# Kernel tuning notes

Measured on AMD Instinct MI355X. Metric: run time of the kernel, lower is better.

The kernel has to match this reference:

```python
import jax, jax.numpy as jnp
import numpy as np

N_NODES = 100000
N_EDGES = 1600000
N_GRAPHS = 512
IN_DIM = 128
HID = 128


def setup_inputs() -> dict:
    key = jax.random.key(0)
    ks = jax.random.split(key, 8)
    x = jax.random.normal(ks[0], (N_NODES, IN_DIM), dtype=jnp.float32)
    edge_index = jax.random.randint(ks[1], (2, N_EDGES), 0, N_NODES, dtype=jnp.int64)
    batch = jnp.sort(jax.random.randint(ks[2], (N_NODES,), 0, N_GRAPHS, dtype=jnp.int64))
    s1 = 1.0 / np.sqrt(IN_DIM)
    s2 = 1.0 / np.sqrt(HID)
    W1 = jax.random.normal(ks[3], (IN_DIM, HID), dtype=jnp.float32) * s1
    b1 = jnp.zeros((HID,), dtype=jnp.float32)
    W2 = jax.random.normal(ks[4], (HID, HID), dtype=jnp.float32) * s2
    b2 = jnp.zeros((HID,), dtype=jnp.float32)
    Wp = jax.random.normal(ks[5], (HID, 1), dtype=jnp.float32) * s2
    bp = jnp.zeros((1,), dtype=jnp.float32)
    return {"x": x, "edge_index": edge_index, "batch": batch,
            "W1": W1, "b1": b1, "W2": W2, "b2": b2, "Wp": Wp, "bp": bp}


def _gcn_conv(x, W, b, src, dst, deg_inv_sqrt):
    # PyG GCNConv: linear transform, then normalized scatter-add (self-loops
    # already appended to src/dst), then bias.
    h = x @ W                                   # [N, H]
    norm = deg_inv_sqrt[src] * deg_inv_sqrt[dst]  # [E+N]
    msg = h[src] * norm[:, None]                # gather + scale
    out = jax.ops.segment_sum(msg, dst, num_segments=N_NODES)
    return out + b


def reference(x, edge_index, batch, W1, b1, W2, b2, Wp, bp):
    # Add self-loops once; degree (with self-loops) over target nodes.
    si = jnp.arange(N_NODES, dtype=edge_index.dtype)
    src = jnp.concatenate([edge_index[0], si])
    dst = jnp.concatenate([edge_index[1], si])
    ones = jnp.ones(src.shape[0], dtype=x.dtype)
    deg = jax.ops.segment_sum(ones, dst, num_segments=N_NODES)
    deg_inv_sqrt = jnp.where(deg > 0, jax.lax.rsqrt(jnp.maximum(deg, 1.0)), 0.0)

    h = jax.nn.relu(_gcn_conv(x, W1, b1, src, dst, deg_inv_sqrt))  # dropout = identity (eval)
    h = jax.nn.relu(_gcn_conv(h, W2, b2, src, dst, deg_inv_sqrt))

    # global_mean_pool over graph ids
    sums = jax.ops.segment_sum(h, batch, num_segments=N_GRAPHS)
    cnts = jax.ops.segment_sum(jnp.ones(N_NODES, dtype=h.dtype), batch, num_segments=N_GRAPHS)
    pooled = sums / jnp.maximum(cnts, 1.0)[:, None]               # [G, H]

    return (pooled @ Wp + bp).squeeze(-1)                          # [G]
```

## Files before the change

kernel.cpp:

```cpp
#include <hip/hip_runtime.h>
#include <hip/hip_bf16.h>

#define NN 100000
#define NG 512
#define H  128

typedef _Float16 half8 __attribute__((ext_vector_type(8)));
typedef float f32x4 __attribute__((ext_vector_type(4)));

__global__ __launch_bounds__(256) void k_wprep_hist(const float* __restrict__ W1,
                                                    const float* __restrict__ W2,
                                                    _Float16* __restrict__ Wt1,
                                                    _Float16* __restrict__ Wt2,
                                                    const int* __restrict__ dst,
                                                    int* __restrict__ deg, int E) {
    int bb = blockIdx.x;
    if (bb < 128) {
        const float* W = (bb < 64) ? W1 : W2;
        _Float16* Wt = (bb < 64) ? Wt1 : Wt2;
        int i = (bb & 63) * 256 + threadIdx.x;
        int k = i >> 7, n = i & 127;
        Wt[n * 128 + k] = (_Float16)W[i];
        return;
    }
    int e = (bb - 128) * 256 + threadIdx.x;
    if (e < E) atomicAdd(&deg[dst[e]], 1);
}

__global__ __launch_bounds__(256) void k_scan_block(const int* __restrict__ deg,
                                                    int* __restrict__ rowptr,
                                                    int* __restrict__ bsum, int n) {
    __shared__ int s[256];
    int tid = threadIdx.x;
    int i = blockIdx.x * 256 + tid;
    int v = (i < n) ? deg[i] : 0;
    s[tid] = v;
    __syncthreads();
    #pragma unroll
    for (int off = 1; off < 256; off <<= 1) {
        int t = (tid >= off) ? s[tid - off] : 0;
        __syncthreads();
        s[tid] += t;
        __syncthreads();
    }
    if (i < n) rowptr[i] = s[tid] - v;
    if (tid == 255) bsum[blockIdx.x] = s[255];
}

__global__ __launch_bounds__(512) void k_scan_top(int* __restrict__ bsum, int nb) {
    __shared__ int s[512];
    int tid = threadIdx.x;
    int v = (tid < nb) ? bsum[tid] : 0;
    s[tid] = v;
    __syncthreads();
    #pragma unroll
    for (int off = 1; off < 512; off <<= 1) {
        int t = (tid >= off) ? s[tid - off] : 0;
        __syncthreads();
        s[tid] += t;
        __syncthreads();
    }
    if (tid < nb) bsum[tid] = s[tid] - v;
}

__global__ __launch_bounds__(256) void k_scan_fin(int* __restrict__ rowptr,
                                                  const int* __restrict__ bsum,
                                                  const int* __restrict__ deg,
                                                  int* __restrict__ cursor,
                                                  float* __restrict__ dinv,
                                                  int n, int E) {
    int i = blockIdx.x * 256 + threadIdx.x;
    if (i >= n) return;
    int r = rowptr[i] + bsum[i >> 8];
    rowptr[i] = r;
    cursor[i] = r;
    dinv[i] = rsqrtf((float)deg[i] + 1.0f);
    if (i == 0) rowptr[n] = E;
}

__global__ __launch_bounds__(256) void k_fill_gemm1(
        const int* __restrict__ src, const int* __restrict__ dst,
        int* __restrict__ cursor, int* __restrict__ col, int E, int nfb,
        const float* __restrict__ x, const _Float16* __restrict__ Wt1,
        const float* __restrict__ dinv, _Float16* __restrict__ tS, int n) {
    if ((int)blockIdx.x < nfb) {
        int e = blockIdx.x * 256 + threadIdx.x;
        if (e >= E) return;
        int d = dst[e];
        int pos = atomicAdd(&cursor[d], 1);
        col[pos] = src[e];
        return;
    }
    const int row0 = ((int)blockIdx.x - nfb) * 64;
    const int tid = threadIdx.x;
    const int w = tid >> 6, lane = tid & 63;
    const int l16 = lane & 15, quad = lane >> 4;
    const int Arow = row0 + w * 16 + l16;
    f32x4 acc[8] = {};
    #pragma unroll
    for (int kk = 0; kk < 4; ++kk) {
        half8 af;
        if (Arow < n) {
            const float* ap = x + (size_t)Arow * H + kk * 32 + quad * 8;
            float4 a0 = ((const float4*)ap)[0];
            float4 a1 = ((const float4*)ap)[1];
            af[0] = (_Float16)a0.x; af[1] = (_Float16)a0.y;
            af[2] = (_Float16)a0.z; af[3] = (_Float16)a0.w;
            af[4] = (_Float16)a1.x; af[5] = (_Float16)a1.y;
            af[6] = (_Float16)a1.z; af[7] = (_Float16)a1.w;
        } else {
            #pragma unroll
            for (int j = 0; j < 8; ++j) af[j] = (_Float16)0.0f;
        }
        #pragma unroll
        for (int nt = 0; nt < 8; ++nt) {
            half8 bf = *((const half8*)(Wt1 + (nt * 16 + l16) * H + kk * 32 + quad * 8));
            acc[nt] = __builtin_amdgcn_mfma_f32_16x16x32_f16(af, bf, acc[nt], 0, 0, 0);
        }
    }
    #pragma unroll
    for (int r = 0; r < 4; ++r) {
        int R = row0 + w * 16 + quad * 4 + r;
        if (R < n) {
            float sc = dinv[R];
            _Float16* crow = tS + (size_t)R * H + l16;
            #pragma unroll
            for (int nt = 0; nt < 8; ++nt)
                crow[nt * 16] = (_Float16)(acc[nt][r] * sc);
        }
    }
}

__global__ __launch_bounds__(256) void k_gemm2(const _Float16* __restrict__ h1,
                                               const _Float16* __restrict__ Wt2,
                                               const float* __restrict__ dinv,
                                               _Float16* __restrict__ tS2, int n) {
    const int row0 = blockIdx.x * 64;
    const int tid = threadIdx.x;
    const int w = tid >> 6, lane = tid & 63;
    const int l16 = lane & 15, quad = lane >> 4;
    const int Arow = row0 + w * 16 + l16;
    f32x4 acc[8] = {};
    #pragma unroll
    for (int kk = 0; kk < 4; ++kk) {
        half8 af;
        if (Arow < n) {
            af = ((const half8*)(h1 + (size_t)Arow * H))[kk * 4 + quad];
        } else {
            #pragma unroll
            for (int j = 0; j < 8; ++j) af[j] = (_Float16)0.0f;
        }
        #pragma unroll
        for (int nt = 0; nt < 8; ++nt) {
            half8 bf = *((const half8*)(Wt2 + (nt * 16 + l16) * H + kk * 32 + quad * 8));
            acc[nt] = __builtin_amdgcn_mfma_f32_16x16x32_f16(af, bf, acc[nt], 0, 0, 0);
        }
    }
    #pragma unroll
    for (int r = 0; r < 4; ++r) {
        int R = row0 + w * 16 + quad * 4 + r;
        if (R < n) {
            float sc = dinv[R];
            _Float16* crow = tS2 + (size_t)R * H + l16;
            #pragma unroll
            for (int nt = 0; nt < 8; ++nt)
                crow[nt * 16] = (_Float16)(acc[nt][r] * sc);
        }
    }
}

__device__ __forceinline__ half8 ld_row16_nol1(const _Float16* p) {
    union { unsigned long long u[2]; half8 h; } t;
    const unsigned long long* q = (const unsigned long long*)p;
    t.u[0] = __hip_atomic_load(q,     __ATOMIC_RELAXED, __HIP_MEMORY_SCOPE_AGENT);
    t.u[1] = __hip_atomic_load(q + 1, __ATOMIC_RELAXED, __HIP_MEMORY_SCOPE_AGENT);
    return t.h;
}

template <bool NOL1>
__device__ __forceinline__ void gather_rows_h(const _Float16* __restrict__ tS,
                                              const int* __restrict__ col,
                                              int node, int e0, int end,
                                              float acc[8]) {
    const int lane = threadIdx.x & 63;
    const int q = lane >> 4;
    const int l16 = lane & 15;
    float a0[8] = {}, a1[8] = {};
    if (q == 0) {
        half8 v = ((const half8*)tS)[(size_t)node * 16 + l16];
        #pragma unroll
        for (int i = 0; i < 8; ++i) a0[i] = (float)v[i];
    }
    for (int base = e0; base < end; base += 64) {
        int ce = base + lane;
        int cidx = (ce < end) ? col[ce] : 0;
        int m = min(64, end - base);
        int nf = m >> 2;
        int g = 0;
        for (; g + 2 <= nf; g += 2) {
            int s0 = __shfl(cidx, 4 * g + q);
            int s1 = __shfl(cidx, 4 * g + 4 + q);
            half8 v0, v1;
            if (NOL1) {
                v0 = ld_row16_nol1(tS + (size_t)s0 * H + l16 * 8);
                v1 = ld_row16_nol1(tS + (size_t)s1 * H + l16 * 8);
            } else {
                v0 = ((const half8*)tS)[(size_t)s0 * 16 + l16];
                v1 = ((const half8*)tS)[(size_t)s1 * 16 + l16];
            }
            #pragma unroll
            for (int i = 0; i < 8; ++i) {
                a0[i] += (float)v0[i];
                a1[i] += (float)v1[i];
            }
        }
        if (g < nf) {
            int s0 = __shfl(cidx, 4 * g + q);
            half8 v0 = NOL1 ? ld_row16_nol1(tS + (size_t)s0 * H + l16 * 8)
                            : ((const half8*)tS)[(size_t)s0 * 16 + l16];
            #pragma unroll
            for (int i = 0; i < 8; ++i) a0[i] += (float)v0[i];
        }
        int tail = m & 3;
        if (tail) {
            int s = __shfl(cidx, 4 * nf + q);
            if (q < tail) {
                half8 v = NOL1 ? ld_row16_nol1(tS + (size_t)s * H + l16 * 8)
                               : ((const half8*)tS)[(size_t)s * 16 + l16];
                #pragma unroll
                for (int i = 0; i < 8; ++i) a0[i] += (float)v[i];
            }
        }
    }
    #pragma unroll
    for (int i = 0; i < 8; ++i) {
        float t = a0[i] + a1[i];
        t += __shfl_xor(t, 16);
        t += __shfl_xor(t, 32);
        acc[i] = t;
    }
}

__global__ __launch_bounds__(256) void k_gather1(const _Float16* __restrict__ tS,
                                                 const int* __restrict__ rowptr,
                                                 const int* __restrict__ col,
                                                 const float* __restrict__ dinv,
                                                 const float* __restrict__ b,
                                                 _Float16* __restrict__ out, int n) {
    int node = blockIdx.x * 4 + (threadIdx.x >> 6);
    int lane = threadIdx.x & 63;
    int q = lane >> 4, l16 = lane & 15;
    if (node >= n) return;
    int e0 = rowptr[node], end = rowptr[node + 1];
    float acc[8];
    gather_rows_h<false>(tS, col, node, e0, end, acc);
    if (q == 0) {
        float dn = dinv[node];
        const float4* b4 = (const float4*)b;
        float4 bb0 = b4[2 * l16], bb1 = b4[2 * l16 + 1];
        half8 hv;
        hv[0] = (_Float16)fmaxf(dn * acc[0] + bb0.x, 0.0f);
        hv[1] = (_Float16)fmaxf(dn * acc[1] + bb0.y, 0.0f);
        hv[2] = (_Float16)fmaxf(dn * acc[2] + bb0.z, 0.0f);
        hv[3] = (_Float16)fmaxf(dn * acc[3] + bb0.w, 0.0f);
        hv[4] = (_Float16)fmaxf(dn * acc[4] + bb1.x, 0.0f);
        hv[5] = (_Float16)fmaxf(dn * acc[5] + bb1.y, 0.0f);
        hv[6] = (_Float16)fmaxf(dn * acc[6] + bb1.z, 0.0f);
        hv[7] = (_Float16)fmaxf(dn * acc[7] + bb1.w, 0.0f);
        ((half8*)out)[(size_t)node * 16 + l16] = hv;
    }
}

__global__ __launch_bounds__(256) void k_gather2(const _Float16* __restrict__ tS,
                                                 const int* __restrict__ rowptr,
                                                 const int* __restrict__ col,
                                                 const float* __restrict__ dinv,
                                                 const float* __restrict__ b,
                                                 const float* __restrict__ Wp,
                                                 const int* __restrict__ batch,
                                                 float* __restrict__ pool,
                                                 float* __restrict__ cnt, int n) {
    int node = blockIdx.x * 4 + (threadIdx.x >> 6);
    int lane = threadIdx.x & 63;
    int l16 = lane & 15;
    if (node >= n) return;
    int e0 = rowptr[node], end = rowptr[node + 1];
    float acc[8];
    gather_rows_h<true>(tS, col, node, e0, end, acc);
    float dn = dinv[node];
    const float4* b4 = (const float4*)b;
    const float4* w4 = (const float4*)Wp;
    float4 bb0 = b4[2 * l16], bb1 = b4[2 * l16 + 1];
    float4 wp0 = w4[2 * l16], wp1 = w4[2 * l16 + 1];
    float s = fmaxf(dn * acc[0] + bb0.x, 0.0f) * wp0.x +
              fmaxf(dn * acc[1] + bb0.y, 0.0f) * wp0.y +
              fmaxf(dn * acc[2] + bb0.z, 0.0f) * wp0.z +
              fmaxf(dn * acc[3] + bb0.w, 0.0f) * wp0.w +
              fmaxf(dn * acc[4] + bb1.x, 0.0f) * wp1.x +
              fmaxf(dn * acc[5] + bb1.y, 0.0f) * wp1.y +
              fmaxf(dn * acc[6] + bb1.z, 0.0f) * wp1.z +
              fmaxf(dn * acc[7] + bb1.w, 0.0f) * wp1.w;
    s += __shfl_xor(s, 1);
    s += __shfl_xor(s, 2);
    s += __shfl_xor(s, 4);
    s += __shfl_xor(s, 8);
    if (lane == 0) {
        int g = batch[node];
        atomicAdd(&pool[g], s);
        atomicAdd(&cnt[g], 1.0f);
    }
}

__global__ __launch_bounds__(256) void final_out_kernel(const float* __restrict__ pool,
                                                        const float* __restrict__ cnt,
                                                        const float* __restrict__ bp,
                                                        float* __restrict__ out, int g) {
    int i = blockIdx.x * 256 + threadIdx.x;
    if (i < g) out[i] = pool[i] / fmaxf(cnt[i], 1.0f) + bp[0];
}

extern "C" void kernel_launch(void* const* d_in, const int* in_sizes, int n_in,
                              void* d_out, int out_size, void* d_ws, size_t ws_size,
                              hipStream_t stream) {
    const float* x     = (const float*)d_in[0];
    const int*   ei    = (const int*)d_in[1];
    const int*   batch = (const int*)d_in[2];
    const float* W1    = (const float*)d_in[3];
    const float* b1    = (const float*)d_in[4];
    const float* W2    = (const float*)d_in[5];
    const float* b2    = (const float*)d_in[6];
    const float* Wp    = (const float*)d_in[7];
    const float* bp    = (const float*)d_in[8];
    float* out = (float*)d_out;

    const int E = in_sizes[1] / 2;
    const int* src = ei;
    const int* dst = ei + E;

    const size_t BUFH = (size_t)NN * H * sizeof(_Float16);
    const size_t NI   = 401408;
    char* ws = (char*)d_ws;
    size_t off = 0;
    _Float16* tS   = (_Float16*)(ws + off); off += BUFH;
    _Float16* h1   = (_Float16*)(ws + off); off += BUFH;
    _Float16* tS2  = (_Float16*)(ws + off); off += BUFH;
    int*      deg  = (int*)     (ws + off); off += NI;
    int*   rowptr  = (int*)     (ws + off); off += NI;
    int*   cursor  = (int*)     (ws + off); off += NI;
    float*    dinv = (float*)   (ws + off); off += NI;
    int*      col  = (int*)     (ws + off); off += ((size_t)E * 4 + 4095) / 4096 * 4096;
    _Float16* Wt1  = (_Float16*)(ws + off); off += 32768;
    _Float16* Wt2  = (_Float16*)(ws + off); off += 32768;
    int*      bsum = (int*)     (ws + off); off += 4096;
    float*    pool = (float*)   (ws + off); off += 2048;
    float*    cnt  = (float*)   (ws + off); off += 2048;

    const int NB  = (NN + 255) / 256;
    const int NFB = (E + 255) / 256;
    const int NGB = (NN + 63) / 64;

    hipMemsetAsync(deg, 0, NN * sizeof(int), stream);
    hipMemsetAsync(pool, 0, 4096, stream);
    k_wprep_hist<<<128 + NFB, 256, 0, stream>>>(W1, W2, Wt1, Wt2, dst, deg, E);
    k_scan_block<<<NB, 256, 0, stream>>>(deg, rowptr, bsum, NN);
    k_scan_top<<<1, 512, 0, stream>>>(bsum, NB);
    k_scan_fin<<<NB, 256, 0, stream>>>(rowptr, bsum, deg, cursor, dinv, NN, E);

    k_fill_gemm1<<<NFB + NGB, 256, 0, stream>>>(src, dst, cursor, col, E, NFB,
                                                x, Wt1, dinv, tS, NN);

    k_gather1<<<(NN + 3) / 4, 256, 0, stream>>>(tS, rowptr, col, dinv, b1, h1, NN);
    k_gemm2<<<NGB, 256, 0, stream>>>(h1, Wt2, dinv, tS2, NN);

    k_gather2<<<(NN + 3) / 4, 256, 0, stream>>>(tS2, rowptr, col, dinv, b2, Wp,
                                                batch, pool, cnt, NN);

    final_out_kernel<<<(NG + 255) / 256, 256, 0, stream>>>(pool, cnt, bp, out, NG);
}
```

Measured before the change: 663.1 us.

## Unroll gather by four rows, use 32-bit offsets, compute graph counts by binary search

Measured after the change: 728.7 us. +9.9%, slower.

```diff
diff --git a/kernel.cpp b/kernel.cpp
--- a/kernel.cpp
+++ b/kernel.cpp
@@ -169,7 +169,7 @@
     }
 }
 
-__device__ __forceinline__ half8 ld_row16_nol1(const _Float16* p) {
+__device__ __forceinline__ half8 ld_row16_nol1(const void* p) {
     union { unsigned long long u[2]; half8 h; } t;
     const unsigned long long* q = (const unsigned long long*)p;
     t.u[0] = __hip_atomic_load(q,     __ATOMIC_RELAXED, __HIP_MEMORY_SCOPE_AGENT);
@@ -185,9 +185,11 @@
     const int lane = threadIdx.x & 63;
     const int q = lane >> 4;
     const int l16 = lane & 15;
+    const char* tSb = (const char*)tS;
+    const uint32_t fo = (uint32_t)(l16 << 4);
     float a0[8] = {}, a1[8] = {};
     if (q == 0) {
-        half8 v = ((const half8*)tS)[(size_t)node * 16 + l16];
+        half8 v = *(const half8*)(tSb + (((uint32_t)node << 8) + fo));
         #pragma unroll
         for (int i = 0; i < 8; ++i) a0[i] = (float)v[i];
     }
@@ -195,40 +197,29 @@
         int ce = base + lane;
         int cidx = (ce < end) ? col[ce] : 0;
         int m = min(64, end - base);
-        int nf = m >> 2;
-        int g = 0;
-        for (; g + 2 <= nf; g += 2) {
-            int s0 = __shfl(cidx, 4 * g + q);
-            int s1 = __shfl(cidx, 4 * g + 4 + q);
-            half8 v0, v1;
+        int ng = (m + 3) >> 2;
+        for (int g = 0; g < ng; g += 4) {
+            int p0 = 4 * g + q, p1 = p0 + 4, p2 = p0 + 8, p3 = p0 + 12;
+            int s0 = __shfl(cidx, p0), s1 = __shfl(cidx, p1);
+            int s2 = __shfl(cidx, p2), s3 = __shfl(cidx, p3);
+            half8 v0 = {}, v1 = {}, v2 = {}, v3 = {};
             if (NOL1) {
-                v0 = ld_row16_nol1(tS + (size_t)s0 * H + l16 * 8);
-                v1 = ld_row16_nol1(tS + (size_t)s1 * H + l16 * 8);
+                if (p0 < m) v0 = ld_row16_nol1(tSb + (((uint32_t)s0 << 8) + fo));
+                if (p1 < m) v1 = ld_row16_nol1(tSb + (((uint32_t)s1 << 8) + fo));
+                if (p2 < m) v2 = ld_row16_nol1(tSb + (((uint32_t)s2 << 8) + fo));
+                if (p3 < m) v3 = ld_row16_nol1(tSb + (((uint32_t)s3 << 8) + fo));
             } else {
-                v0 = ((const half8*)tS)[(size_t)s0 * 16 + l16];
-                v1 = ((const half8*)tS)[(size_t)s1 * 16 + l16];
+                if (p0 < m) v0 = *(const half8*)(tSb + (((uint32_t)s0 << 8) + fo));
+                if (p1 < m) v1 = *(const half8*)(tSb + (((uint32_t)s1 << 8) + fo));
+                if (p2 < m) v2 = *(const half8*)(tSb + (((uint32_t)s2 << 8) + fo));
+                if (p3 < m) v3 = *(const half8*)(tSb + (((uint32_t)s3 << 8) + fo));
             }
             #pragma unroll
             for (int i = 0; i < 8; ++i) {
                 a0[i] += (float)v0[i];
                 a1[i] += (float)v1[i];
-            }
-        }
-        if (g < nf) {
-            int s0 = __shfl(cidx, 4 * g + q);
-            half8 v0 = NOL1 ? ld_row16_nol1(tS + (size_t)s0 * H + l16 * 8)
-                            : ((const half8*)tS)[(size_t)s0 * 16 + l16];
-            #pragma unroll
-            for (int i = 0; i < 8; ++i) a0[i] += (float)v0[i];
-        }
-        int tail = m & 3;
-        if (tail) {
-            int s = __shfl(cidx, 4 * nf + q);
-            if (q < tail) {
-                half8 v = NOL1 ? ld_row16_nol1(tS + (size_t)s * H + l16 * 8)
-                               : ((const half8*)tS)[(size_t)s * 16 + l16];
-                #pragma unroll
-                for (int i = 0; i < 8; ++i) a0[i] += (float)v[i];
+                a0[i] += (float)v2[i];
+                a1[i] += (float)v3[i];
             }
         }
     }
@@ -278,8 +269,7 @@
                                                  const float* __restrict__ b,
                                                  const float* __restrict__ Wp,
                                                  const int* __restrict__ batch,
-                                                 float* __restrict__ pool,
-                                                 float* __restrict__ cnt, int n) {
+                                                 float* __restrict__ pool, int n) {
     int node = blockIdx.x * 4 + (threadIdx.x >> 6);
     int lane = threadIdx.x & 63;
     int l16 = lane & 15;
@@ -307,16 +297,22 @@
     if (lane == 0) {
         int g = batch[node];
         atomicAdd(&pool[g], s);
-        atomicAdd(&cnt[g], 1.0f);
     }
 }
 
 __global__ __launch_bounds__(256) void final_out_kernel(const float* __restrict__ pool,
-                                                        const float* __restrict__ cnt,
+                                                        const int* __restrict__ batch,
                                                         const float* __restrict__ bp,
                                                         float* __restrict__ out, int g) {
     int i = blockIdx.x * 256 + threadIdx.x;
-    if (i < g) out[i] = pool[i] / fmaxf(cnt[i], 1.0f) + bp[0];
+    if (i >= g) return;
+    int lo = 0, hi = NN;
+    while (lo < hi) { int mid = (lo + hi) >> 1; if (batch[mid] < i) lo = mid + 1; else hi = mid; }
+    int s0 = lo;
+    hi = NN;
+    while (lo < hi) { int mid = (lo + hi) >> 1; if (batch[mid] < i + 1) lo = mid + 1; else hi = mid; }
+    float c = (float)(lo - s0);
+    out[i] = pool[i] / fmaxf(c, 1.0f) + bp[0];
 }
 
 extern "C" void kernel_launch(void* const* d_in, const int* in_sizes, int n_in,
@@ -353,14 +349,13 @@
     _Float16* Wt2  = (_Float16*)(ws + off); off += 32768;
     int*      bsum = (int*)     (ws + off); off += 4096;
     float*    pool = (float*)   (ws + off); off += 2048;
-    float*    cnt  = (float*)   (ws + off); off += 2048;
 
     const int NB  = (NN + 255) / 256;
     const int NFB = (E + 255) / 256;
     const int NGB = (NN + 63) / 64;
 
     hipMemsetAsync(deg, 0, NN * sizeof(int), stream);
-    hipMemsetAsync(pool, 0, 4096, stream);
+    hipMemsetAsync(pool, 0, 2048, stream);
     k_wprep_hist<<<128 + NFB, 256, 0, stream>>>(W1, W2, Wt1, Wt2, dst, deg, E);
     k_scan_block<<<NB, 256, 0, stream>>>(deg, rowptr, bsum, NN);
     k_scan_top<<<1, 512, 0, stream>>>(bsum, NB);
@@ -373,7 +368,7 @@
     k_gemm2<<<NGB, 256, 0, stream>>>(h1, Wt2, dinv, tS2, NN);
 
     k_gather2<<<(NN + 3) / 4, 256, 0, stream>>>(tS2, rowptr, col, dinv, b2, Wp,
-                                                batch, pool, cnt, NN);
-
-    final_out_kernel<<<(NG + 255) / 256, 256, 0, stream>>>(pool, cnt, bp, out, NG);
-}
+                                                batch, pool, NN);
+
+    final_out_kernel<<<(NG + 255) / 256, 256, 0, stream>>>(pool, batch, bp, out, NG);
+}
```

## Split edge gathers into feature-column slices to shrink the random-access working set

Applied to the files above, without the earlier changes.

Result: slower. 1.530 ms (+130.7%).

```diff
diff --git a/kernel.cpp b/kernel.cpp
--- a/kernel.cpp
+++ b/kernel.cpp
@@ -5,7 +5,9 @@
 #define NG 512
 #define H  128
 
-typedef _Float16 half8 __attribute__((ext_vector_type(8)));
+typedef _Float16 half8  __attribute__((ext_vector_type(8)));
+typedef _Float16 half4v __attribute__((ext_vector_type(4)));
+typedef _Float16 half2v __attribute__((ext_vector_type(2)));
 typedef float f32x4 __attribute__((ext_vector_type(4)));
 
 __global__ __launch_bounds__(256) void k_wprep_hist(const float* __restrict__ W1,
@@ -169,27 +171,46 @@
     }
 }
 
-__device__ __forceinline__ half8 ld_row16_nol1(const _Float16* p) {
-    union { unsigned long long u[2]; half8 h; } t;
-    const unsigned long long* q = (const unsigned long long*)p;
-    t.u[0] = __hip_atomic_load(q,     __ATOMIC_RELAXED, __HIP_MEMORY_SCOPE_AGENT);
-    t.u[1] = __hip_atomic_load(q + 1, __ATOMIC_RELAXED, __HIP_MEMORY_SCOPE_AGENT);
-    return t.h;
-}
-
-template <bool NOL1>
-__device__ __forceinline__ void gather_rows_h(const _Float16* __restrict__ tS,
+template <int F, bool NOL1>
+__device__ __forceinline__ void frag_load(const char* p, float* t) {
+    if constexpr (F == 4) {
+        union { unsigned long long u; half4v h; } c;
+        if constexpr (NOL1) {
+            c.u = __hip_atomic_load((const unsigned long long*)p,
+                                    __ATOMIC_RELAXED, __HIP_MEMORY_SCOPE_AGENT);
+        } else {
+            c.h = *(const half4v*)p;
+        }
+        t[0] = (float)c.h[0]; t[1] = (float)c.h[1];
+        t[2] = (float)c.h[2]; t[3] = (float)c.h[3];
+    } else {
+        union { unsigned int u; half2v h; } c;
+        if constexpr (NOL1) {
+            c.u = __hip_atomic_load((const unsigned int*)p,
+                                    __ATOMIC_RELAXED, __HIP_MEMORY_SCOPE_AGENT);
+        } else {
+            c.h = *(const half2v*)p;
+        }
+        t[0] = (float)c.h[0]; t[1] = (float)c.h[1];
+    }
+}
+
+template <int F, bool NOL1>
+__device__ __forceinline__ void gather_rows_f(const _Float16* __restrict__ tS,
                                               const int* __restrict__ col,
-                                              int node, int e0, int end,
-                                              float acc[8]) {
+                                              int node, int e0, int end, int hoffB,
+                                              float acc[F]) {
     const int lane = threadIdx.x & 63;
     const int q = lane >> 4;
     const int l16 = lane & 15;
-    float a0[8] = {}, a1[8] = {};
+    const char* tSb = (const char*)tS;
+    const uint32_t fo = (uint32_t)(hoffB + l16 * (F * 2));
+    float a0[F] = {}, a1[F] = {};
     if (q == 0) {
-        half8 v = ((const half8*)tS)[(size_t)node * 16 + l16];
+        float t[F];
+        frag_load<F, false>(tSb + (((uint32_t)node << 8) + fo), t);
         #pragma unroll
-        for (int i = 0; i < 8; ++i) a0[i] = (float)v[i];
+        for (int i = 0; i < F; ++i) a0[i] = t[i];
     }
     for (int base = e0; base < end; base += 64) {
         int ce = base + lane;
@@ -200,40 +221,35 @@
         for (; g + 2 <= nf; g += 2) {
             int s0 = __shfl(cidx, 4 * g + q);
             int s1 = __shfl(cidx, 4 * g + 4 + q);
-            half8 v0, v1;
-            if (NOL1) {
-                v0 = ld_row16_nol1(tS + (size_t)s0 * H + l16 * 8);
-                v1 = ld_row16_nol1(tS + (size_t)s1 * H + l16 * 8);
-            } else {
-                v0 = ((const half8*)tS)[(size_t)s0 * 16 + l16];
-                v1 = ((const half8*)tS)[(size_t)s1 * 16 + l16];
-            }
-            #pragma unroll
-            for (int i = 0; i < 8; ++i) {
-                a0[i] += (float)v0[i];
-                a1[i] += (float)v1[i];
+            float t0[F], t1[F];
+            frag_load<F, NOL1>(tSb + (((uint32_t)s0 << 8) + fo), t0);
+            frag_load<F, NOL1>(tSb + (((uint32_t)s1 << 8) + fo), t1);
+            #pragma unroll
+            for (int i = 0; i < F; ++i) {
+                a0[i] += t0[i];
+                a1[i] += t1[i];
             }
         }
         if (g < nf) {
             int s0 = __shfl(cidx, 4 * g + q);
-            half8 v0 = NOL1 ? ld_row16_nol1(tS + (size_t)s0 * H + l16 * 8)
-                            : ((const half8*)tS)[(size_t)s0 * 16 + l16];
-            #pragma unroll
-            for (int i = 0; i < 8; ++i) a0[i] += (float)v0[i];
+            float t0[F];
+            frag_load<F, NOL1>(tSb + (((uint32_t)s0 << 8) + fo), t0);
+            #pragma unroll
+            for (int i = 0; i < F; ++i) a0[i] += t0[i];
         }
         int tail = m & 3;
         if (tail) {
             int s = __shfl(cidx, 4 * nf + q);
             if (q < tail) {
-                half8 v = NOL1 ? ld_row16_nol1(tS + (size_t)s * H + l16 * 8)
-                               : ((const half8*)tS)[(size_t)s * 16 + l16];
+                float t[F];
+                frag_load<F, NOL1>(tSb + (((uint32_t)s << 8) + fo), t);
                 #pragma unroll
-                for (int i = 0; i < 8; ++i) a0[i] += (float)v[i];
+                for (int i = 0; i < F; ++i) a0[i] += t[i];
             }
         }
     }
     #pragma unroll
-    for (int i = 0; i < 8; ++i) {
+    for (int i = 0; i < F; ++i) {
         float t = a0[i] + a1[i];
         t += __shfl_xor(t, 16);
         t += __shfl_xor(t, 32);
@@ -246,28 +262,25 @@
                                                  const int* __restrict__ col,
                                                  const float* __restrict__ dinv,
                                                  const float* __restrict__ b,
-                                                 _Float16* __restrict__ out, int n) {
+                                                 _Float16* __restrict__ out,
+                                                 int n, int hoff) {
     int node = blockIdx.x * 4 + (threadIdx.x >> 6);
     int lane = threadIdx.x & 63;
     int q = lane >> 4, l16 = lane & 15;
     if (node >= n) return;
     int e0 = rowptr[node], end = rowptr[node + 1];
-    float acc[8];
-    gather_rows_h<false>(tS, col, node, e0, end, acc);
+    const int hoffB = hoff * 2;
+    float acc[4];
+    gather_rows_f<4, false>(tS, col, node, e0, end, hoffB, acc);
     if (q == 0) {
         float dn = dinv[node];
-        const float4* b4 = (const float4*)b;
-        float4 bb0 = b4[2 * l16], bb1 = b4[2 * l16 + 1];
-        half8 hv;
-        hv[0] = (_Float16)fmaxf(dn * acc[0] + bb0.x, 0.0f);
-        hv[1] = (_Float16)fmaxf(dn * acc[1] + bb0.y, 0.0f);
-        hv[2] = (_Float16)fmaxf(dn * acc[2] + bb0.z, 0.0f);
-        hv[3] = (_Float16)fmaxf(dn * acc[3] + bb0.w, 0.0f);
-        hv[4] = (_Float16)fmaxf(dn * acc[4] + bb1.x, 0.0f);
-        hv[5] = (_Float16)fmaxf(dn * acc[5] + bb1.y, 0.0f);
-        hv[6] = (_Float16)fmaxf(dn * acc[6] + bb1.z, 0.0f);
-        hv[7] = (_Float16)fmaxf(dn * acc[7] + bb1.w, 0.0f);
-        ((half8*)out)[(size_t)node * 16 + l16] = hv;
+        float4 bb = ((const float4*)b)[(hoff >> 2) + l16];
+        half4v hv;
+        hv[0] = (_Float16)fmaxf(dn * acc[0] + bb.x, 0.0f);
+        hv[1] = (_Float16)fmaxf(dn * acc[1] + bb.y, 0.0f);
+        hv[2] = (_Float16)fmaxf(dn * acc[2] + bb.z, 0.0f);
+        hv[3] = (_Float16)fmaxf(dn * acc[3] + bb.w, 0.0f);
+        *(half4v*)((char*)out + (((size_t)node << 8) + hoffB + l16 * 8)) = hv;
     }
 }
 
@@ -279,27 +292,20 @@
                                                  const float* __restrict__ Wp,
                                                  const int* __restrict__ batch,
                                                  float* __restrict__ pool,
-                                                 float* __restrict__ cnt, int n) {
+                                                 int n, int hoff) {
     int node = blockIdx.x * 4 + (threadIdx.x >> 6);
     int lane = threadIdx.x & 63;
     int l16 = lane & 15;
     if (node >= n) return;
     int e0 = rowptr[node], end = rowptr[node + 1];
-    float acc[8];
-    gather_rows_h<true>(tS, col, node, e0, end, acc);
+    const int hoffB = hoff * 2;
+    float acc[2];
+    gather_rows_f<2, true>(tS, col, node, e0, end, hoffB, acc);
     float dn = dinv[node];
-    const float4* b4 = (const float4*)b;
-    const float4* w4 = (const float4*)Wp;
-    float4 bb0 = b4[2 * l16], bb1 = b4[2 * l16 + 1];
-    float4 wp0 = w4[2 * l16], wp1 = w4[2 * l16 + 1];
-    float s = fmaxf(dn * acc[0] + bb0.x, 0.0f) * wp0.x +
-              fmaxf(dn * acc[1] + bb0.y, 0.0f) * wp0.y +
-              fmaxf(dn * acc[2] + bb0.z, 0.0f) * wp0.z +
-              fmaxf(dn * acc[3] + bb0.w, 0.0f) * wp0.w +
-              fmaxf(dn * acc[4] + bb1.x, 0.0f) * wp1.x +
-              fmaxf(dn * acc[5] + bb1.y, 0.0f) * wp1.y +
-              fmaxf(dn * acc[6] + bb1.z, 0.0f) * wp1.z +
-              fmaxf(dn * acc[7] + bb1.w, 0.0f) * wp1.w;
+    float2 bb = ((const float2*)b)[(hoff >> 1) + l16];
+    float2 wp = ((const float2*)Wp)[(hoff >> 1) + l16];
+    float s = fmaxf(dn * acc[0] + bb.x, 0.0f) * wp.x +
+              fmaxf(dn * acc[1] + bb.y, 0.0f) * wp.y;
     s += __shfl_xor(s, 1);
     s += __shfl_xor(s, 2);
     s += __shfl_xor(s, 4);
@@ -307,16 +313,22 @@
     if (lane == 0) {
         int g = batch[node];
         atomicAdd(&pool[g], s);
-        atomicAdd(&cnt[g], 1.0f);
     }
 }
 
 __global__ __launch_bounds__(256) void final_out_kernel(const float* __restrict__ pool,
-                                                        const float* __restrict__ cnt,
+                                                        const int* __restrict__ batch,
                                                         const float* __restrict__ bp,
                                                         float* __restrict__ out, int g) {
     int i = blockIdx.x * 256 + threadIdx.x;
-    if (i < g) out[i] = pool[i] / fmaxf(cnt[i], 1.0f) + bp[0];
+    if (i >= g) return;
+    int lo = 0, hi = NN;
+    while (lo < hi) { int mid = (lo + hi) >> 1; if (batch[mid] < i) lo = mid + 1; else hi = mid; }
+    int s0 = lo;
+    hi = NN;
+    while (lo < hi) { int mid = (lo + hi) >> 1; if (batch[mid] < i + 1) lo = mid + 1; else hi = mid; }
+    float c = (float)(lo - s0);
+    out[i] = pool[i] / fmaxf(c, 1.0f) + bp[0];
 }
 
 extern "C" void kernel_launch(void* const* d_in, const int* in_sizes, int n_in,
@@ -353,14 +365,14 @@
     _Float16* Wt2  = (_Float16*)(ws + off); off += 32768;
     int*      bsum = (int*)     (ws + off); off += 4096;
     float*    pool = (float*)   (ws + off); off += 2048;
-    float*    cnt  = (float*)   (ws + off); off += 2048;
 
     const int NB  = (NN + 255) / 256;
     const int NFB = (E + 255) / 256;
     const int NGB = (NN + 63) / 64;
+    const int NGA = (NN + 3) / 4;
 
     hipMemsetAsync(deg, 0, NN * sizeof(int), stream);
-    hipMemsetAsync(pool, 0, 4096, stream);
+    hipMemsetAsync(pool, 0, 2048, stream);
     k_wprep_hist<<<128 + NFB, 256, 0, stream>>>(W1, W2, Wt1, Wt2, dst, deg, E);
     k_scan_block<<<NB, 256, 0, stream>>>(deg, rowptr, bsum, NN);
     k_scan_top<<<1, 512, 0, stream>>>(bsum, NB);
@@ -369,11 +381,14 @@
     k_fill_gemm1<<<NFB + NGB, 256, 0, stream>>>(src, dst, cursor, col, E, NFB,
                                                 x, Wt1, dinv, tS, NN);
 
-    k_gather1<<<(NN + 3) / 4, 256, 0, stream>>>(tS, rowptr, col, dinv, b1, h1, NN);
+    k_gather1<<<NGA, 256, 0, stream>>>(tS, rowptr, col, dinv, b1, h1, NN, 0);
+    k_gather1<<<NGA, 256, 0, stream>>>(tS, rowptr, col, dinv, b1, h1, NN, 64);
     k_gemm2<<<NGB, 256, 0, stream>>>(h1, Wt2, dinv, tS2, NN);
 
-    k_gather2<<<(NN + 3) / 4, 256, 0, stream>>>(tS2, rowptr, col, dinv, b2, Wp,
-                                                batch, pool, cnt, NN);
-
-    final_out_kernel<<<(NG + 255) / 256, 256, 0, stream>>>(pool, cnt, bp, out, NG);
-}
+    k_gather2<<<NGA, 256, 0, stream>>>(tS2, rowptr, col, dinv, b2, Wp, batch, pool, NN, 0);
+    k_gather2<<<NGA, 256, 0, stream>>>(tS2, rowptr, col, dinv, b2, Wp, batch, pool, NN, 32);
+    k_gather2<<<NGA, 256, 0, stream>>>(tS2, rowptr, col, dinv, b2, Wp, batch, pool, NN, 64);
+    k_gather2<<<NGA, 256, 0, stream>>>(tS2, rowptr, col, dinv, b2, Wp, batch, pool, NN, 96);
+
+    final_out_kernel<<<(NG + 255) / 256, 256, 0, stream>>>(pool, batch, bp, out, NG);
+}
```

## Process two nodes per wavefront in gathers and derive graph counts by binary search

Applied to the files above, without the earlier changes.

Measured after the change: 692.4 us. 4.4% more time.

```diff
diff --git a/kernel.cpp b/kernel.cpp
--- a/kernel.cpp
+++ b/kernel.cpp
@@ -178,10 +178,10 @@
 }
 
 template <bool NOL1>
-__device__ __forceinline__ void gather_rows_h(const _Float16* __restrict__ tS,
-                                              const int* __restrict__ col,
-                                              int node, int e0, int end,
-                                              float acc[8]) {
+__device__ __forceinline__ void gather_core(const _Float16* __restrict__ tS,
+                                            const int* __restrict__ col,
+                                            int node, int e0, int end, int cidx,
+                                            float acc[8]) {
     const int lane = threadIdx.x & 63;
     const int q = lane >> 4;
     const int l16 = lane & 15;
@@ -192,8 +192,10 @@
         for (int i = 0; i < 8; ++i) a0[i] = (float)v[i];
     }
     for (int base = e0; base < end; base += 64) {
-        int ce = base + lane;
-        int cidx = (ce < end) ? col[ce] : 0;
+        if (base != e0) {
+            int ce = base + lane;
+            cidx = (ce < end) ? col[ce] : 0;
+        }
         int m = min(64, end - base);
         int nf = m >> 2;
         int g = 0;
@@ -241,23 +243,30 @@
     }
 }
 
-__global__ __launch_bounds__(256) void k_gather1(const _Float16* __restrict__ tS,
+__global__ __launch_bounds__(512) void k_gather1(const _Float16* __restrict__ tS,
                                                  const int* __restrict__ rowptr,
                                                  const int* __restrict__ col,
                                                  const float* __restrict__ dinv,
                                                  const float* __restrict__ b,
                                                  _Float16* __restrict__ out, int n) {
-    int node = blockIdx.x * 4 + (threadIdx.x >> 6);
+    int half = (n + 1) >> 1;
+    int widx = blockIdx.x * 8 + (threadIdx.x >> 6);
+    if (widx >= half) return;
+    int nA = widx, nB = widx + half;
+    bool hasB = (nB < n);
     int lane = threadIdx.x & 63;
     int q = lane >> 4, l16 = lane & 15;
-    if (node >= n) return;
-    int e0 = rowptr[node], end = rowptr[node + 1];
+    int e0A = rowptr[nA], e1A = rowptr[nA + 1];
+    int e0B = hasB ? rowptr[nB] : 0;
+    int e1B = hasB ? rowptr[nB + 1] : 0;
+    int cA = (e0A + lane < e1A) ? col[e0A + lane] : 0;
+    int cB = (e0B + lane < e1B) ? col[e0B + lane] : 0;
+    const float4* b4 = (const float4*)b;
+    float4 bb0 = b4[2 * l16], bb1 = b4[2 * l16 + 1];
     float acc[8];
-    gather_rows_h<false>(tS, col, node, e0, end, acc);
+    gather_core<false>(tS, col, nA, e0A, e1A, cA, acc);
     if (q == 0) {
-        float dn = dinv[node];
-        const float4* b4 = (const float4*)b;
-        float4 bb0 = b4[2 * l16], bb1 = b4[2 * l16 + 1];
+        float dn = dinv[nA];
         half8 hv;
         hv[0] = (_Float16)fmaxf(dn * acc[0] + bb0.x, 0.0f);
         hv[1] = (_Float16)fmaxf(dn * acc[1] + bb0.y, 0.0f);
@@ -267,56 +276,100 @@
         hv[5] = (_Float16)fmaxf(dn * acc[5] + bb1.y, 0.0f);
         hv[6] = (_Float16)fmaxf(dn * acc[6] + bb1.z, 0.0f);
         hv[7] = (_Float16)fmaxf(dn * acc[7] + bb1.w, 0.0f);
-        ((half8*)out)[(size_t)node * 16 + l16] = hv;
-    }
-}
-
-__global__ __launch_bounds__(256) void k_gather2(const _Float16* __restrict__ tS,
+        ((half8*)out)[(size_t)nA * 16 + l16] = hv;
+    }
+    if (hasB) {
+        gather_core<false>(tS, col, nB, e0B, e1B, cB, acc);
+        if (q == 0) {
+            float dn = dinv[nB];
+            half8 hv;
+            hv[0] = (_Float16)fmaxf(dn * acc[0] + bb0.x, 0.0f);
+            hv[1] = (_Float16)fmaxf(dn * acc[1] + bb0.y, 0.0f);
+            hv[2] = (_Float16)fmaxf(dn * acc[2] + bb0.z, 0.0f);
+            hv[3] = (_Float16)fmaxf(dn * acc[3] + bb0.w, 0.0f);
+            hv[4] = (_Float16)fmaxf(dn * acc[4] + bb1.x, 0.0f);
+            hv[5] = (_Float16)fmaxf(dn * acc[5] + bb1.y, 0.0f);
+            hv[6] = (_Float16)fmaxf(dn * acc[6] + bb1.z, 0.0f);
+            hv[7] = (_Float16)fmaxf(dn * acc[7] + bb1.w, 0.0f);
+            ((half8*)out)[(size_t)nB * 16 + l16] = hv;
+        }
+    }
+}
+
+__global__ __launch_bounds__(512) void k_gather2(const _Float16* __restrict__ tS,
                                                  const int* __restrict__ rowptr,
                                                  const int* __restrict__ col,
                                                  const float* __restrict__ dinv,
                                                  const float* __restrict__ b,
                                                  const float* __restrict__ Wp,
                                                  const int* __restrict__ batch,
-                                                 float* __restrict__ pool,
-                                                 float* __restrict__ cnt, int n) {
-    int node = blockIdx.x * 4 + (threadIdx.x >> 6);
+                                                 float* __restrict__ pool, int n) {
+    int half = (n + 1) >> 1;
+    int widx = blockIdx.x * 8 + (threadIdx.x >> 6);
+    if (widx >= half) return;
+    int nA = widx, nB = widx + half;
+    bool hasB = (nB < n);
     int lane = threadIdx.x & 63;
     int l16 = lane & 15;
-    if (node >= n) return;
-    int e0 = rowptr[node], end = rowptr[node + 1];
-    float acc[8];
-    gather_rows_h<true>(tS, col, node, e0, end, acc);
-    float dn = dinv[node];
+    int e0A = rowptr[nA], e1A = rowptr[nA + 1];
+    int e0B = hasB ? rowptr[nB] : 0;
+    int e1B = hasB ? rowptr[nB + 1] : 0;
+    int cA = (e0A + lane < e1A) ? col[e0A + lane] : 0;
+    int cB = (e0B + lane < e1B) ? col[e0B + lane] : 0;
     const float4* b4 = (const float4*)b;
     const float4* w4 = (const float4*)Wp;
     float4 bb0 = b4[2 * l16], bb1 = b4[2 * l16 + 1];
     float4 wp0 = w4[2 * l16], wp1 = w4[2 * l16 + 1];
-    float s = fmaxf(dn * acc[0] + bb0.x, 0.0f) * wp0.x +
-              fmaxf(dn * acc[1] + bb0.y, 0.0f) * wp0.y +
-              fmaxf(dn * acc[2] + bb0.z, 0.0f) * wp0.z +
-              fmaxf(dn * acc[3] + bb0.w, 0.0f) * wp0.w +
-              fmaxf(dn * acc[4] + bb1.x, 0.0f) * wp1.x +
-              fmaxf(dn * acc[5] + bb1.y, 0.0f) * wp1.y +
-              fmaxf(dn * acc[6] + bb1.z, 0.0f) * wp1.z +
-              fmaxf(dn * acc[7] + bb1.w, 0.0f) * wp1.w;
-    s += __shfl_xor(s, 1);
-    s += __shfl_xor(s, 2);
-    s += __shfl_xor(s, 4);
-    s += __shfl_xor(s, 8);
-    if (lane == 0) {
-        int g = batch[node];
-        atomicAdd(&pool[g], s);
-        atomicAdd(&cnt[g], 1.0f);
+    float acc[8];
+    gather_core<true>(tS, col, nA, e0A, e1A, cA, acc);
+    {
+        float dn = dinv[nA];
+        float s = fmaxf(dn * acc[0] + bb0.x, 0.0f) * wp0.x +
+                  fmaxf(dn * acc[1] + bb0.y, 0.0f) * wp0.y +
+                  fmaxf(dn * acc[2] + bb0.z, 0.0f) * wp0.z +
+                  fmaxf(dn * acc[3] + bb0.w, 0.0f) * wp0.w +
+                  fmaxf(dn * acc[4] + bb1.x, 0.0f) * wp1.x +
+                  fmaxf(dn * acc[5] + bb1.y, 0.0f) * wp1.y +
+                  fmaxf(dn * acc[6] + bb1.z, 0.0f) * wp1.z +
+                  fmaxf(dn * acc[7] + bb1.w, 0.0f) * wp1.w;
+        s += __shfl_xor(s, 1);
+        s += __shfl_xor(s, 2);
+        s += __shfl_xor(s, 4);
+        s += __shfl_xor(s, 8);
+        if (lane == 0) atomicAdd(&pool[batch[nA]], s);
+    }
+    if (hasB) {
+        gather_core<true>(tS, col, nB, e0B, e1B, cB, acc);
+        float dn = dinv[nB];
+        float s = fmaxf(dn * acc[0] + bb0.x, 0.0f) * wp0.x +
+                  fmaxf(dn * acc[1] + bb0.y, 0.0f) * wp0.y +
+                  fmaxf(dn * acc[2] + bb0.z, 0.0f) * wp0.z +
+                  fmaxf(dn * acc[3] + bb0.w, 0.0f) * wp0.w +
+                  fmaxf(dn * acc[4] + bb1.x, 0.0f) * wp1.x +
+                  fmaxf(dn * acc[5] + bb1.y, 0.0f) * wp1.y +
+                  fmaxf(dn * acc[6] + bb1.z, 0.0f) * wp1.z +
+                  fmaxf(dn * acc[7] + bb1.w, 0.0f) * wp1.w;
+        s += __shfl_xor(s, 1);
+        s += __shfl_xor(s, 2);
+        s += __shfl_xor(s, 4);
+        s += __shfl_xor(s, 8);
+        if (lane == 0) atomicAdd(&pool[batch[nB]], s);
     }
 }
 
 __global__ __launch_bounds__(256) void final_out_kernel(const float* __restrict__ pool,
-                                                        const float* __restrict__ cnt,
+                                                        const int* __restrict__ batch,
                                                         const float* __restrict__ bp,
                                                         float* __restrict__ out, int g) {
     int i = blockIdx.x * 256 + threadIdx.x;
-    if (i < g) out[i] = pool[i] / fmaxf(cnt[i], 1.0f) + bp[0];
+    if (i >= g) return;
+    int lo = 0, hi = NN;
+    while (lo < hi) { int mid = (lo + hi) >> 1; if (batch[mid] < i) lo = mid + 1; else hi = mid; }
+    int s0 = lo;
+    hi = NN;
+    while (lo < hi) { int mid = (lo + hi) >> 1; if (batch[mid] < i + 1) lo = mid + 1; else hi = mid; }
+    float c = (float)(lo - s0);
+    out[i] = pool[i] / fmaxf(c, 1.0f) + bp[0];
 }
 
 extern "C" void kernel_launch(void* const* d_in, const int* in_sizes, int n_in,
@@ -353,14 +406,15 @@
     _Float16* Wt2  = (_Float16*)(ws + off); off += 32768;
     int*      bsum = (int*)     (ws + off); off += 4096;
     float*    pool = (float*)   (ws + off); off += 2048;
-    float*    cnt  = (float*)   (ws + off); off += 2048;
 
     const int NB  = (NN + 255) / 256;
     const int NFB = (E + 255) / 256;
     const int NGB = (NN + 63) / 64;
+    const int HALF = (NN + 1) / 2;
+    const int NGA = (HALF + 7) / 8;
 
     hipMemsetAsync(deg, 0, NN * sizeof(int), stream);
-    hipMemsetAsync(pool, 0, 4096, stream);
+    hipMemsetAsync(pool, 0, 2048, stream);
     k_wprep_hist<<<128 + NFB, 256, 0, stream>>>(W1, W2, Wt1, Wt2, dst, deg, E);
     k_scan_block<<<NB, 256, 0, stream>>>(deg, rowptr, bsum, NN);
     k_scan_top<<<1, 512, 0, stream>>>(bsum, NB);
@@ -369,11 +423,11 @@
     k_fill_gemm1<<<NFB + NGB, 256, 0, stream>>>(src, dst, cursor, col, E, NFB,
                                                 x, Wt1, dinv, tS, NN);
 
-    k_gather1<<<(NN + 3) / 4, 256, 0, stream>>>(tS, rowptr, col, dinv, b1, h1, NN);
+    k_gather1<<<NGA, 512, 0, stream>>>(tS, rowptr, col, dinv, b1, h1, NN);
     k_gemm2<<<NGB, 256, 0, stream>>>(h1, Wt2, dinv, tS2, NN);
 
-    k_gather2<<<(NN + 3) / 4, 256, 0, stream>>>(tS2, rowptr, col, dinv, b2, Wp,
-                                                batch, pool, cnt, NN);
-
-    final_out_kernel<<<(NG + 255) / 256, 256, 0, stream>>>(pool, cnt, bp, out, NG);
-}
+    k_gather2<<<NGA, 512, 0, stream>>>(tS2, rowptr, col, dinv, b2, Wp,
+                                       batch, pool, NN);
+
+    final_out_kernel<<<(NG + 255) / 256, 256, 0, stream>>>(pool, batch, bp, out, NG);
+}
```
